# Performance work log

Hardware: AMD Instinct MI355X
Metric: run time of the kernel (lower is better)

## Reference

```python
import jax, jax.numpy as jnp
import numpy as np

D = 128
N = 8192

def setup_inputs() -> dict:
    key = jax.random.key(0)
    k1, k2, k3 = jax.random.split(key, 3)
    return {
        "query": jax.random.normal(k1, (D, N), dtype=jnp.float32),
        "key": jax.random.normal(k2, (D, N), dtype=jnp.float32),
        "value": jax.random.normal(k3, (D, N), dtype=jnp.float32),
    }

def reference(query, key, value):
    # query, key, value: [d, N] (feature-major, as in the torch module)
    # scores[q, k] = sum_d query[d, q] * key[d, k]  -- NOTE: unscaled (no 1/sqrt(d))
    scores = jnp.einsum("dq,dk->qk", query, key)          # [Nq, Nk]
    p_attn = jax.nn.softmax(scores, axis=-1)               # [Nq, Nk]
    p_val = jnp.einsum("qk,dk->dq", p_attn, value)        # [d, Nq]
    return p_val
```

## Files before the change

### kernel.cpp

```cpp
#include <hip/hip_runtime.h>

#define NN 8192
#define DD 128
#define KSPLIT 16
#define KCHUNK (NN / KSPLIT)
#define BK 32
#define NT (KCHUNK / BK)
#define NTILES (NN / BK)
#define TILE_B 16384
#define OFF_V 8192
#define WAVES 4
#define BQ (WAVES * 32)

#define WS_M   ((size_t)NTILES * TILE_B)
#define WS_L   (WS_M + (size_t)KSPLIT * NN * 4)
#define WS_OP  (WS_L + (size_t)KSPLIT * NN * 4)
#define WS_NEED (WS_OP + (size_t)KSPLIT * NN * DD * 2)

typedef __attribute__((ext_vector_type(8))) _Float16 f16x8;
typedef __attribute__((ext_vector_type(2))) _Float16 f16x2;
typedef __attribute__((ext_vector_type(8))) short bf16x8;
typedef __attribute__((ext_vector_type(4))) float f32x4;
typedef __attribute__((ext_vector_type(2))) float f32x2;
typedef __attribute__((ext_vector_type(16))) float f32x16;

static __device__ __forceinline__ unsigned short f2bf(float f) {
    union { float f; unsigned u; } v; v.f = f;
    return (unsigned short)((v.u + 0x7FFFu + ((v.u >> 16) & 1u)) >> 16);
}
static __device__ __forceinline__ float bf2f(unsigned short h) {
    union { unsigned u; float f; } v; v.u = ((unsigned)h) << 16;
    return v.f;
}
static __device__ __forceinline__ void gld_lds16(const char* g, char* l) {
    __builtin_amdgcn_global_load_lds(
        (const __attribute__((address_space(1))) unsigned*)g,
        (__attribute__((address_space(3))) unsigned*)l,
        16, 0, 0);
}

__global__ __launch_bounds__(256) void attn_prep(
    const float* __restrict__ Km, const float* __restrict__ Vm,
    char* __restrict__ kst)
{
    __shared__ __align__(16) char img[TILE_B];
    const int tt = blockIdx.x;
    const int tid = threadIdx.x;
    const int k0 = tt * BK;
    #pragma unroll
    for (int i = 0; i < 16; ++i) {
        int idx = i * 256 + tid;
        int d = idx >> 5, k = idx & 31;
        float kv = Km[(size_t)d * NN + k0 + k];
        int b = (k * 256 + d * 2) ^ ((k & 7) << 4);
        *(_Float16*)(img + b) = (_Float16)kv;
    }
    #pragma unroll
    for (int i = 0; i < 16; ++i) {
        int idx = i * 256 + tid;
        int d = idx >> 5, j = idx & 31;
        int kl = (j & 3) + 4 * ((j >> 3) & 1) + 8 * ((j >> 2) & 1) + 16 * (j >> 4);
        float vv = Vm[(size_t)d * NN + k0 + kl];
        int b = (d * 64 + j * 2) ^ ((d & 7) << 4);
        *(_Float16*)(img + OFF_V + b) = (_Float16)vv;
    }
    __syncthreads();
    float4* dst = (float4*)(kst + (size_t)tt * TILE_B);
    const float4* src = (const float4*)img;
    #pragma unroll
    for (int i = 0; i < 4; ++i) dst[i * 256 + tid] = src[i * 256 + tid];
}

__global__ __launch_bounds__(256, 3) void attn_main(
    const float* __restrict__ Qm, const char* __restrict__ kst,
    float* __restrict__ mArr, float* __restrict__ lArr,
    _Float16* __restrict__ opart)
{
    __shared__ __align__(16) char smem[2 * TILE_B];
    const int tid = threadIdx.x;
    const int wave = tid >> 6, lane = tid & 63;
    const int q31 = lane & 31;
    const int h = lane >> 5;
    const int swz = (lane & 7) << 4;
    const int ks = blockIdx.x & (KSPLIT - 1);
    const int qb = blockIdx.x >> 4;
    const int q0w = qb * BQ + wave * 32;
    const int qg = q0w + q31;
    const float LOG2E = 1.44269504088896340736f;

    f16x8 qh[8];
    #pragma unroll
    for (int ds = 0; ds < 8; ++ds)
        #pragma unroll
        for (int jj = 0; jj < 8; ++jj) {
            int d = 16 * ds + 8 * h + jj;
            qh[ds][jj] = (_Float16)(Qm[(size_t)d * NN + qg] * LOG2E);
        }

    f32x16 acc[4];
    #pragma unroll
    for (int dt = 0; dt < 4; ++dt)
        #pragma unroll
        for (int r = 0; r < 16; ++r) acc[dt][r] = 0.f;
    float mrun = -INFINITY, lrun = 0.f;

    {
        const char* gsrc = kst + (size_t)(ks * NT) * TILE_B + tid * 16;
        char* ldst = smem + tid * 16;
        #pragma unroll
        for (int i = 0; i < 4; ++i) gld_lds16(gsrc + i * 4096, ldst + i * 4096);
    }
    __syncthreads();

    for (int t = 0; t < NT; ++t) {
        const int cur = t & 1;
        const char* kb = smem + cur * TILE_B;

        if (t + 1 < NT) {
            const char* gsrc = kst + (size_t)(ks * NT + t + 1) * TILE_B + tid * 16;
            char* ldst = smem + (cur ^ 1) * TILE_B + tid * 16;
            #pragma unroll
            for (int i = 0; i < 4; ++i) gld_lds16(gsrc + i * 4096, ldst + i * 4096);
        }

        f32x16 T;
        #pragma unroll
        for (int r = 0; r < 16; ++r) T[r] = 0.f;
        __builtin_amdgcn_s_setprio(1);
        #pragma unroll
        for (int ds = 0; ds < 8; ++ds) {
            int off = ((q31 << 8) + ds * 32 + (h << 4)) ^ swz;
            f16x8 kh = *(const f16x8*)(kb + off);
            T = __builtin_amdgcn_mfma_f32_32x32x16_f16(kh, qh[ds], T, 0, 0, 0);
        }
        __builtin_amdgcn_s_setprio(0);

        float tmax = fmaxf(T[0], T[1]);
        #pragma unroll
        for (int r = 2; r < 16; ++r) tmax = fmaxf(tmax, T[r]);
        tmax = fmaxf(tmax, __shfl_xor(tmax, 32, 64));

        if (__any(tmax > mrun)) {
            float mnew = fmaxf(mrun, tmax);
            float sc = __builtin_amdgcn_exp2f(mrun - mnew);
            mrun = mnew;
            lrun *= sc;
            #pragma unroll
            for (int dt = 0; dt < 4; ++dt)
                #pragma unroll
                for (int r = 0; r < 16; ++r) acc[dt][r] *= sc;
        }

        f16x8 pfrag[2];
        float psum = 0.f;
        #pragma unroll
        for (int s2 = 0; s2 < 2; ++s2)
            #pragma unroll
            for (int jj = 0; jj < 8; ++jj) {
                float p = __builtin_amdgcn_exp2f(T[8 * s2 + jj] - mrun);
                psum += p;
                pfrag[s2][jj] = (_Float16)p;
            }
        lrun += psum;

        __builtin_amdgcn_s_setprio(1);
        #pragma unroll
        for (int dt = 0; dt < 4; ++dt) {
            int vbase = (dt * 32 + q31) * 64 + (h << 4);
            #pragma unroll
            for (int s2 = 0; s2 < 2; ++s2) {
                f16x8 vb = *(const f16x8*)(kb + OFF_V + ((vbase + s2 * 32) ^ swz));
                acc[dt] = __builtin_amdgcn_mfma_f32_32x32x16_f16(vb, pfrag[s2], acc[dt], 0, 0, 0);
            }
        }
        __builtin_amdgcn_s_setprio(0);

        __syncthreads();
    }

    lrun += __shfl_xor(lrun, 32, 64);
    if (lane < 32) {
        mArr[ks * NN + qg] = mrun;
        lArr[ks * NN + qg] = lrun;
    }
    #pragma unroll
    for (int dt = 0; dt < 4; ++dt)
        #pragma unroll
        for (int r = 0; r < 16; ++r) {
            int d = dt * 32 + (r & 3) + 8 * (r >> 2) + 4 * h;
            opart[((size_t)ks * DD + d) * NN + qg] = (_Float16)acc[dt][r];
        }
}

__global__ __launch_bounds__(256) void attn_combine(
    const _Float16* __restrict__ opart, const float* __restrict__ mArr,
    const float* __restrict__ lArr, float* __restrict__ out)
{
    const int tid = threadIdx.x;
    const int qg = blockIdx.x >> 3;
    const int dseg = (blockIdx.x & 7) * 16;
    const int q = qg * 512 + tid * 2;

    f32x2 mv[KSPLIT];
    float M0 = -INFINITY, M1 = -INFINITY;
    #pragma unroll
    for (int s = 0; s < KSPLIT; ++s) {
        mv[s] = *(const f32x2*)&mArr[(size_t)s * NN + q];
        M0 = fmaxf(M0, mv[s][0]);
        M1 = fmaxf(M1, mv[s][1]);
    }
    float L0 = 0.f, L1 = 0.f;
    f32x2 w[KSPLIT];
    #pragma unroll
    for (int s = 0; s < KSPLIT; ++s) {
        f32x2 lv = *(const f32x2*)&lArr[(size_t)s * NN + q];
        w[s][0] = __builtin_amdgcn_exp2f(mv[s][0] - M0);
        w[s][1] = __builtin_amdgcn_exp2f(mv[s][1] - M1);
        L0 += w[s][0] * lv[0];
        L1 += w[s][1] * lv[1];
    }
    float i0 = 1.f / L0, i1 = 1.f / L1;
    #pragma unroll
    for (int s = 0; s < KSPLIT; ++s) { w[s][0] *= i0; w[s][1] *= i1; }

    for (int dd = 0; dd < 16; ++dd) {
        int d = dseg + dd;
        float a0 = 0.f, a1 = 0.f;
        #pragma unroll
        for (int s = 0; s < KSPLIT; ++s) {
            f16x2 u = *(const f16x2*)&opart[((size_t)s * DD + d) * NN + q];
            a0 += w[s][0] * (float)u[0];
            a1 += w[s][1] * (float)u[1];
        }
        f32x2 o; o[0] = a0; o[1] = a1;
        *(f32x2*)&out[(size_t)d * NN + q] = o;
    }
}

__global__ __launch_bounds__(512, 2) void attn_fwd_fb(
    const float* __restrict__ Qm, const float* __restrict__ Km,
    const float* __restrict__ Vm, float* __restrict__ out)
{
    const int tid  = threadIdx.x;
    const int wave = tid >> 6;
    const int lane = tid & 63;
    const int c = lane & 15;
    const int g = lane >> 4;
    const int q0 = blockIdx.x * 32;
    const float LOG2E = 1.44269504088896340736f;

    bf16x8 qhi[2][4], qlo[2][4];
    #pragma unroll
    for (int qt = 0; qt < 2; ++qt)
        #pragma unroll
        for (int ds = 0; ds < 4; ++ds)
            #pragma unroll
            for (int jj = 0; jj < 8; ++jj) {
                int d = ds * 32 + 8 * g + jj;
                float qv = Qm[(size_t)d * NN + (q0 + qt * 16 + c)] * LOG2E;
                unsigned short hv = f2bf(qv);
                qhi[qt][ds][jj] = (short)hv;
                qlo[qt][ds][jj] = (short)f2bf(qv - bf2f(hv));
            }

    f32x4 acc[2][8];
    #pragma unroll
    for (int a = 0; a < 2; ++a)
        #pragma unroll
        for (int b = 0; b < 8; ++b)
            acc[a][b] = (f32x4){0.f, 0.f, 0.f, 0.f};
    float mrun[2] = {-INFINITY, -INFINITY};
    float lrun[2] = {0.f, 0.f};
    const int kw0 = wave * (NN / 8);

    for (int t = 0; t < (NN / 8) / 64; ++t) {
        const int k0 = kw0 + t * 64;
        f32x4 T[4][2];
        #pragma unroll
        for (int mkt = 0; mkt < 4; ++mkt) {
            T[mkt][0] = (f32x4){0.f, 0.f, 0.f, 0.f};
            T[mkt][1] = (f32x4){0.f, 0.f, 0.f, 0.f};
        }
        #pragma unroll
        for (int mkt = 0; mkt < 4; ++mkt) {
            const int kc = k0 + mkt * 16 + c;
            #pragma unroll
            for (int ds = 0; ds < 4; ++ds) {
                bf16x8 khi, klo;
                #pragma unroll
                for (int jj = 0; jj < 8; ++jj) {
                    int d = ds * 32 + 8 * g + jj;
                    float kv = Km[(size_t)d * NN + kc];
                    unsigned short hv = f2bf(kv);
                    khi[jj] = (short)hv;
                    klo[jj] = (short)f2bf(kv - bf2f(hv));
                }
                #pragma unroll
                for (int qt = 0; qt < 2; ++qt) {
                    T[mkt][qt] = __builtin_amdgcn_mfma_f32_16x16x32_bf16(khi, qhi[qt][ds], T[mkt][qt], 0, 0, 0);
                    T[mkt][qt] = __builtin_amdgcn_mfma_f32_16x16x32_bf16(khi, qlo[qt][ds], T[mkt][qt], 0, 0, 0);
                    T[mkt][qt] = __builtin_amdgcn_mfma_f32_16x16x32_bf16(klo, qhi[qt][ds], T[mkt][qt], 0, 0, 0);
                }
            }
        }
        bf16x8 pfrag[2][2];
        float scl[2];
        #pragma unroll
        for (int qt = 0; qt < 2; ++qt) {
            float tmax = T[0][qt][0];
            #pragma unroll
            for (int mkt = 0; mkt < 4; ++mkt)
                #pragma unroll
                for (int r = 0; r < 4; ++r)
                    tmax = fmaxf(tmax, T[mkt][qt][r]);
            tmax = fmaxf(tmax, __shfl_xor(tmax, 16, 64));
            tmax = fmaxf(tmax, __shfl_xor(tmax, 32, 64));
            float mnew = fmaxf(mrun[qt], tmax);
            float sc = __builtin_amdgcn_exp2f(mrun[qt] - mnew);
            mrun[qt] = mnew;
            lrun[qt] *= sc;
            scl[qt] = sc;
            #pragma unroll
            for (int s = 0; s < 2; ++s)
                #pragma unroll
                for (int hf = 0; hf < 2; ++hf) {
                    int mkt = 2 * s + hf;
                    #pragma unroll
                    for (int r = 0; r < 4; ++r) {
                        float p = __builtin_amdgcn_exp2f(T[mkt][qt][r] - mnew);
                        unsigned short pb = f2bf(p);
                        lrun[qt] += bf2f(pb);
                        pfrag[qt][s][hf * 4 + r] = (short)pb;
                    }
                }
        }
        #pragma unroll
        for (int qt = 0; qt < 2; ++qt)
            #pragma unroll
            for (int r = 0; r < 4; ++r) {
                float f = __shfl(scl[qt], 4 * g + r, 64);
                #pragma unroll
                for (int dt = 0; dt < 8; ++dt)
                    acc[qt][dt][r] *= f;
            }
        #pragma unroll
        for (int s = 0; s < 2; ++s)
            #pragma unroll
            for (int dt = 0; dt < 8; ++dt) {
                const float* vp = Vm + (size_t)(dt * 16 + c) * NN + (k0 + 32 * s + 4 * g);
                f32x4 v0 = *(const f32x4*)vp;
                f32x4 v1 = *(const f32x4*)(vp + 16);
                bf16x8 vb;
                #pragma unroll
                for (int e = 0; e < 4; ++e) {
                    vb[e]     = (short)f2bf(v0[e]);
                    vb[4 + e] = (short)f2bf(v1[e]);
                }
                #pragma unroll
                for (int qt = 0; qt < 2; ++qt)
                    acc[qt][dt] = __builtin_amdgcn_mfma_f32_16x16x32_bf16(pfrag[qt][s], vb, acc[qt][dt], 0, 0, 0);
            }
    }

    __shared__ float obuf[32][DD + 4];
    __shared__ float mbuf[8][32];
    __shared__ float lbuf[8][32];
    __shared__ float lsbuf[32];
    #pragma unroll
    for (int qt = 0; qt < 2; ++qt) {
        lrun[qt] += __shfl_xor(lrun[qt], 16, 64);
        lrun[qt] += __shfl_xor(lrun[qt], 32, 64);
    }
    if (lane < 16) {
        mbuf[wave][c]      = mrun[0];
        mbuf[wave][16 + c] = mrun[1];
        lbuf[wave][c]      = lrun[0];
        lbuf[wave][16 + c] = lrun[1];
    }
    for (int i = tid; i < 32 * (DD + 4); i += 512)
        (&obuf[0][0])[i] = 0.f;
    __syncthreads();
    float fac[2];
    {
        float lst[2];
        #pragma unroll
        for (int qt = 0; qt < 2; ++qt) {
            int q = qt * 16 + c;
            float mm = -INFINITY;
            #pragma unroll
            for (int w = 0; w < 8; ++w) mm = fmaxf(mm, mbuf[w][q]);
            float ls = 0.f;
            #pragma unroll
            for (int w = 0; w < 8; ++w)
                ls += __builtin_amdgcn_exp2f(mbuf[w][q] - mm) * lbuf[w][q];
            fac[qt] = __builtin_amdgcn_exp2f(mrun[qt] - mm);
            lst[qt] = ls;
        }
        if (wave == 0 && lane < 16) {
            lsbuf[c]      = lst[0];
            lsbuf[16 + c] = lst[1];
        }
    }
    float facr[2][4];
    #pragma unroll
    for (int qt = 0; qt < 2; ++qt)
        #pragma unroll
        for (int r = 0; r < 4; ++r)
            facr[qt][r] = __shfl(fac[qt], 4 * g + r, 64);
    for (int w = 0; w < 8; ++w) {
        if (wave == w) {
            #pragma unroll
            for (int qt = 0; qt < 2; ++qt)
                #pragma unroll
                for (int dt = 0; dt < 8; ++dt)
                    #pragma unroll
                    for (int r = 0; r < 4; ++r)
                        obuf[qt * 16 + 4 * g + r][dt * 16 + c] += facr[qt][r] * acc[qt][dt][r];
        }
        __syncthreads();
    }
    const int qq = tid & 31;
    const int dg = tid >> 5;
    const float inv = 1.f / lsbuf[qq];
    #pragma unroll
    for (int i = 0; i < 8; ++i) {
        int d = dg * 8 + i;
        out[(size_t)d * NN + q0 + qq] = obuf[qq][d] * inv;
    }
}

extern "C" void kernel_launch(void* const* d_in, const int* in_sizes, int n_in,
                              void* d_out, int out_size, void* d_ws, size_t ws_size,
                              hipStream_t stream) {
    const float* Q = (const float*)d_in[0];
    const float* K = (const float*)d_in[1];
    const float* V = (const float*)d_in[2];
    float* out = (float*)d_out;

    if (ws_size < WS_NEED || d_ws == nullptr) {
        hipLaunchKernelGGL(attn_fwd_fb, dim3(NN / 32), dim3(512), 0, stream, Q, K, V, out);
        return;
    }
    char* ws = (char*)d_ws;
    char* kst = ws;
    float* mArr = (float*)(ws + WS_M);
    float* lArr = (float*)(ws + WS_L);
    _Float16* opart = (_Float16*)(ws + WS_OP);

    hipLaunchKernelGGL(attn_prep, dim3(NTILES), dim3(256), 0, stream, K, V, kst);
    hipLaunchKernelGGL(attn_main, dim3(KSPLIT * (NN / BQ)), dim3(256), 0, stream, Q, kst, mArr, lArr, opart);
    hipLaunchKernelGGL(attn_combine, dim3((NN / 512) * 8), dim3(256), 0, stream, opart, mArr, lArr, out);
}
```

Baseline: 71.15 us.

## Software-pipeline QK of next tile with softmax/PV, deepen LDS staging, halve K-split

Restructures the main attention loop into a 4-deep LDS ring with prefetch two tiles ahead, computing the QK MFMA for tile t+1 before the softmax and PV of tile t so matrix and exp work can overlap. Also halves the K-split count (fewer partial outputs to write and combine, longer per-block loops), widens the K-tile swizzle to 16 rows, and uses packed fp16 conversion with tree reductions. This costs more LDS and registers (occupancy hint lowered to 2) and fewer blocks in the grid.

```diff
diff --git a/kernel.cpp b/kernel.cpp
--- a/kernel.cpp
+++ b/kernel.cpp
@@ -2,7 +2,7 @@
 
 #define NN 8192
 #define DD 128
-#define KSPLIT 16
+#define KSPLIT 8
 #define KCHUNK (NN / KSPLIT)
 #define BK 32
 #define NT (KCHUNK / BK)
@@ -19,6 +19,7 @@
 
 typedef __attribute__((ext_vector_type(8))) _Float16 f16x8;
 typedef __attribute__((ext_vector_type(2))) _Float16 f16x2;
+typedef __attribute__((ext_vector_type(2))) __fp16 fp16v2;
 typedef __attribute__((ext_vector_type(8))) short bf16x8;
 typedef __attribute__((ext_vector_type(4))) float f32x4;
 typedef __attribute__((ext_vector_type(2))) float f32x2;
@@ -52,7 +53,7 @@
         int idx = i * 256 + tid;
         int d = idx >> 5, k = idx & 31;
         float kv = Km[(size_t)d * NN + k0 + k];
-        int b = (k * 256 + d * 2) ^ ((k & 7) << 4);
+        int b = (k * 256 + d * 2) ^ ((k & 15) << 4);
         *(_Float16*)(img + b) = (_Float16)kv;
     }
     #pragma unroll
@@ -71,19 +72,20 @@
     for (int i = 0; i < 4; ++i) dst[i * 256 + tid] = src[i * 256 + tid];
 }
 
-__global__ __launch_bounds__(256, 3) void attn_main(
+__global__ __launch_bounds__(256, 2) void attn_main(
     const float* __restrict__ Qm, const char* __restrict__ kst,
     float* __restrict__ mArr, float* __restrict__ lArr,
     _Float16* __restrict__ opart)
 {
-    __shared__ __align__(16) char smem[2 * TILE_B];
+    __shared__ __align__(16) char smem[4 * TILE_B];
     const int tid = threadIdx.x;
     const int wave = tid >> 6, lane = tid & 63;
     const int q31 = lane & 31;
     const int h = lane >> 5;
-    const int swz = (lane & 7) << 4;
+    const int kswz = (q31 & 15) << 4;
+    const int vswz = (lane & 7) << 4;
     const int ks = blockIdx.x & (KSPLIT - 1);
-    const int qb = blockIdx.x >> 4;
+    const int qb = blockIdx.x >> 3;
     const int q0w = qb * BQ + wave * 32;
     const int qg = q0w + q31;
     const float LOG2E = 1.44269504088896340736f;
@@ -104,78 +106,98 @@
         for (int r = 0; r < 16; ++r) acc[dt][r] = 0.f;
     float mrun = -INFINITY, lrun = 0.f;
 
-    {
-        const char* gsrc = kst + (size_t)(ks * NT) * TILE_B + tid * 16;
-        char* ldst = smem + tid * 16;
-        #pragma unroll
-        for (int i = 0; i < 4; ++i) gld_lds16(gsrc + i * 4096, ldst + i * 4096);
-    }
+    const char* kwg = kst + (size_t)(ks * NT) * TILE_B + tid * 16;
+
+#define STAGE(T, BI)                                                        \
+    {                                                                       \
+        const char* gs_ = kwg + (size_t)(T) * TILE_B;                       \
+        char* ld_ = smem + (BI) * TILE_B + tid * 16;                        \
+        gld_lds16(gs_,          ld_);                                       \
+        gld_lds16(gs_ + 4096,   ld_ + 4096);                                \
+        gld_lds16(gs_ + 8192,   ld_ + 8192);                                \
+        gld_lds16(gs_ + 12288,  ld_ + 12288);                               \
+    }
+
+#define QKSTEP(BI, TDST)                                                    \
+    {                                                                       \
+        const char* kb_ = smem + (BI) * TILE_B;                             \
+        _Pragma("unroll")                                                   \
+        for (int r = 0; r < 16; ++r) TDST[r] = 0.f;                         \
+        __builtin_amdgcn_s_setprio(1);                                      \
+        _Pragma("unroll")                                                   \
+        for (int ds = 0; ds < 8; ++ds) {                                    \
+            int off_ = ((q31 << 8) + ds * 32 + (h << 4)) ^ kswz;            \
+            f16x8 kh_ = *(const f16x8*)(kb_ + off_);                        \
+            TDST = __builtin_amdgcn_mfma_f32_32x32x16_f16(kh_, qh[ds], TDST, 0, 0, 0); \
+        }                                                                   \
+        __builtin_amdgcn_s_setprio(0);                                      \
+    }
+
+#define SMPV(BI, TCUR)                                                      \
+    {                                                                       \
+        float a0_ = fmaxf(fmaxf(TCUR[0], TCUR[1]), TCUR[2]);                \
+        float a1_ = fmaxf(fmaxf(TCUR[3], TCUR[4]), TCUR[5]);                \
+        float a2_ = fmaxf(fmaxf(TCUR[6], TCUR[7]), TCUR[8]);                \
+        float a3_ = fmaxf(fmaxf(TCUR[9], TCUR[10]), TCUR[11]);              \
+        float a4_ = fmaxf(fmaxf(TCUR[12], TCUR[13]), TCUR[14]);             \
+        float tmax_ = fmaxf(fmaxf(fmaxf(a0_, a1_), a2_),                    \
+                            fmaxf(fmaxf(a3_, a4_), TCUR[15]));              \
+        tmax_ = fmaxf(tmax_, __shfl_xor(tmax_, 32, 64));                    \
+        if (__any(tmax_ > mrun)) {                                          \
+            float mnew_ = fmaxf(mrun, tmax_);                               \
+            float sc_ = __builtin_amdgcn_exp2f(mrun - mnew_);               \
+            mrun = mnew_; lrun *= sc_;                                      \
+            _Pragma("unroll")                                               \
+            for (int dt = 0; dt < 4; ++dt)                                  \
+                _Pragma("unroll")                                           \
+                for (int r = 0; r < 16; ++r) acc[dt][r] *= sc_;             \
+        }                                                                   \
+        float p_[16];                                                       \
+        _Pragma("unroll")                                                   \
+        for (int r = 0; r < 16; ++r)                                        \
+            p_[r] = __builtin_amdgcn_exp2f(TCUR[r] - mrun);                 \
+        float s0_ = (p_[0] + p_[1]) + (p_[2] + p_[3]);                      \
+        float s1_ = (p_[4] + p_[5]) + (p_[6] + p_[7]);                      \
+        float s2_ = (p_[8] + p_[9]) + (p_[10] + p_[11]);                    \
+        float s3_ = (p_[12] + p_[13]) + (p_[14] + p_[15]);                  \
+        lrun += (s0_ + s1_) + (s2_ + s3_);                                  \
+        union { f16x8 v[2]; fp16v2 h2[8]; } pu_;                            \
+        _Pragma("unroll")                                                   \
+        for (int r = 0; r < 8; ++r)                                         \
+            pu_.h2[r] = __builtin_amdgcn_cvt_pkrtz(p_[2 * r], p_[2 * r + 1]); \
+        const char* vb_ = smem + (BI) * TILE_B + OFF_V;                     \
+        __builtin_amdgcn_s_setprio(1);                                      \
+        _Pragma("unroll")                                                   \
+        for (int dt = 0; dt < 4; ++dt) {                                    \
+            int vbase_ = (dt * 32 + q31) * 64 + (h << 4);                   \
+            f16x8 v0_ = *(const f16x8*)(vb_ + ((vbase_) ^ vswz));           \
+            f16x8 v1_ = *(const f16x8*)(vb_ + ((vbase_ + 32) ^ vswz));      \
+            acc[dt] = __builtin_amdgcn_mfma_f32_32x32x16_f16(v0_, pu_.v[0], acc[dt], 0, 0, 0); \
+            acc[dt] = __builtin_amdgcn_mfma_f32_32x32x16_f16(v1_, pu_.v[1], acc[dt], 0, 0, 0); \
+        }                                                                   \
+        __builtin_amdgcn_s_setprio(0);                                      \
+    }
+
+#define STEP(I, TCUR, TNXT)                                                 \
+    {                                                                       \
+        const int t_ = tb + (I);                                            \
+        if (t_ + 2 < NT) STAGE(t_ + 2, ((I) + 2) & 3);                      \
+        if (t_ + 1 < NT) QKSTEP(((I) + 1) & 3, TNXT);                       \
+        SMPV((I) & 3, TCUR);                                                \
+        __syncthreads();                                                    \
+    }
+
+    STAGE(0, 0);
+    STAGE(1, 1);
     __syncthreads();
-
-    for (int t = 0; t < NT; ++t) {
-        const int cur = t & 1;
-        const char* kb = smem + cur * TILE_B;
-
-        if (t + 1 < NT) {
-            const char* gsrc = kst + (size_t)(ks * NT + t + 1) * TILE_B + tid * 16;
-            char* ldst = smem + (cur ^ 1) * TILE_B + tid * 16;
-            #pragma unroll
-            for (int i = 0; i < 4; ++i) gld_lds16(gsrc + i * 4096, ldst + i * 4096);
-        }
-
-        f32x16 T;
-        #pragma unroll
-        for (int r = 0; r < 16; ++r) T[r] = 0.f;
-        __builtin_amdgcn_s_setprio(1);
-        #pragma unroll
-        for (int ds = 0; ds < 8; ++ds) {
-            int off = ((q31 << 8) + ds * 32 + (h << 4)) ^ swz;
-            f16x8 kh = *(const f16x8*)(kb + off);
-            T = __builtin_amdgcn_mfma_f32_32x32x16_f16(kh, qh[ds], T, 0, 0, 0);
-        }
-        __builtin_amdgcn_s_setprio(0);
-
-        float tmax = fmaxf(T[0], T[1]);
-        #pragma unroll
-        for (int r = 2; r < 16; ++r) tmax = fmaxf(tmax, T[r]);
-        tmax = fmaxf(tmax, __shfl_xor(tmax, 32, 64));
-
-        if (__any(tmax > mrun)) {
-            float mnew = fmaxf(mrun, tmax);
-            float sc = __builtin_amdgcn_exp2f(mrun - mnew);
-            mrun = mnew;
-            lrun *= sc;
-            #pragma unroll
-            for (int dt = 0; dt < 4; ++dt)
-                #pragma unroll
-                for (int r = 0; r < 16; ++r) acc[dt][r] *= sc;
-        }
-
-        f16x8 pfrag[2];
-        float psum = 0.f;
-        #pragma unroll
-        for (int s2 = 0; s2 < 2; ++s2)
-            #pragma unroll
-            for (int jj = 0; jj < 8; ++jj) {
-                float p = __builtin_amdgcn_exp2f(T[8 * s2 + jj] - mrun);
-                psum += p;
-                pfrag[s2][jj] = (_Float16)p;
-            }
-        lrun += psum;
-
-        __builtin_amdgcn_s_setprio(1);
-        #pragma unroll
-        for (int dt = 0; dt < 4; ++dt) {
-            int vbase = (dt * 32 + q31) * 64 + (h << 4);
-            #pragma unroll
-            for (int s2 = 0; s2 < 2; ++s2) {
-                f16x8 vb = *(const f16x8*)(kb + OFF_V + ((vbase + s2 * 32) ^ swz));
-                acc[dt] = __builtin_amdgcn_mfma_f32_32x32x16_f16(vb, pfrag[s2], acc[dt], 0, 0, 0);
-            }
-        }
-        __builtin_amdgcn_s_setprio(0);
-
-        __syncthreads();
+    f32x16 TA, TB;
+    QKSTEP(0, TA);
+
+    for (int tb = 0; tb < NT; tb += 4) {
+        STEP(0, TA, TB);
+        STEP(1, TB, TA);
+        STEP(2, TA, TB);
+        STEP(3, TB, TA);
     }
 
     lrun += __shfl_xor(lrun, 32, 64);
@@ -190,6 +212,10 @@
             int d = dt * 32 + (r & 3) + 8 * (r >> 2) + 4 * h;
             opart[((size_t)ks * DD + d) * NN + qg] = (_Float16)acc[dt][r];
         }
+#undef STAGE
+#undef QKSTEP
+#undef SMPV
+#undef STEP
 }
 
 __global__ __launch_bounds__(256) void attn_combine(
```

Result: faster. 65.63 us (-7.8%).
